# Optimization experiments

Measured on AMD Instinct MI355X. Metric: run time of the kernel, lower is better.

## Reference

```python
import jax, jax.numpy as jnp
import numpy as np

EPS = 1e-8  # torch.cosine_similarity clamps norms at eps=1e-8


def setup_inputs() -> dict:
    key = jax.random.key(0)
    k1, k2, k3 = jax.random.split(key, 3)
    B, C, D = 256, 128, 1024
    return {
        "doc_emb": jax.random.normal(k1, (B, D), dtype=jnp.float32),
        "summary_emb": jax.random.normal(k2, (B, D), dtype=jnp.float32),
        "candidate_emb": jax.random.normal(k3, (B, C, D), dtype=jnp.float32),
    }


def _clamped_norm(x):
    return jnp.maximum(jnp.linalg.norm(x, axis=-1), EPS)


def reference(doc_emb, summary_emb, candidate_emb):
    # doc_emb: [B, D], summary_emb: [B, D], candidate_emb: [B, C, D]
    B, C, D = candidate_emb.shape
    dn = _clamped_norm(doc_emb)          # [B]
    sn = _clamped_norm(summary_emb)      # [B]
    cn = _clamped_norm(candidate_emb)    # [B, C]

    # outer_score[b,c] = cos(candidate[b,c], doc[b])
    outer_score = jnp.einsum("bcd,bd->bc", candidate_emb, doc_emb) / (cn * dn[:, None])

    # inner_score: replaces the O(B*C^2) python loop with one batched Gram matmul.
    chat = candidate_emb / cn[:, :, None]           # unit candidates [B, C, D]
    gram = jnp.einsum("bcd,bkd->bck", chat, chat)    # [B, C, C] cosine sims
    diag = jnp.einsum("bcc->bc", gram)               # self-similarity (==1)
    inner_score = (gram.sum(axis=-1) - diag) / (C - 1)  # mean over _cn != cn

    # summary_score[b] = cos(summary[b], doc[b])
    summary_score = jnp.einsum("bd,bd->b", summary_emb, doc_emb) / (sn * dn)

    # summary_avg_score[b] = mean_c cos(summary[b], candidate[b,c])
    sc = jnp.einsum("bd,bcd->bc", summary_emb, candidate_emb) / (sn[:, None] * cn)
    summary_avg_score = sc.mean(axis=-1)

    return (outer_score, inner_score, summary_score, summary_avg_score)
```

## Files before the change

kernel.cpp:

```cpp
#include <hip/hip_runtime.h>
#include <math.h>


#define EPS 1e-8f
constexpr int B = 256;
constexpr int C = 128;
constexpr int D = 1024;

__device__ __forceinline__ float waveReduceSum(float v) {
    v += __shfl_down(v, 32, 64);
    v += __shfl_down(v, 16, 64);
    v += __shfl_down(v, 8, 64);
    v += __shfl_down(v, 4, 64);
    v += __shfl_down(v, 2, 64);
    v += __shfl_down(v, 1, 64);
    return v;
}

__global__ __launch_bounds__(256) void k0_norms(
    const float* __restrict__ doc, const float* __restrict__ summ,
    float* __restrict__ dn_inv, float* __restrict__ sn_inv,
    float* __restrict__ out_sumscore, float* __restrict__ out_sumavg) {
    const int b = blockIdx.x;
    const int t = threadIdx.x;
    const float4 dv = ((const float4*)(doc + (size_t)b * D))[t];
    const float4 sv = ((const float4*)(summ + (size_t)b * D))[t];
    float dd = dv.x * dv.x + dv.y * dv.y + dv.z * dv.z + dv.w * dv.w;
    float ss = sv.x * sv.x + sv.y * sv.y + sv.z * sv.z + sv.w * sv.w;
    float sd = sv.x * dv.x + sv.y * dv.y + sv.z * dv.z + sv.w * dv.w;
    dd = waveReduceSum(dd);
    ss = waveReduceSum(ss);
    sd = waveReduceSum(sd);
    __shared__ float red[3][4];
    const int wave = t >> 6, lane = t & 63;
    if (lane == 0) { red[0][wave] = dd; red[1][wave] = ss; red[2][wave] = sd; }
    __syncthreads();
    if (t == 0) {
        const float DD = red[0][0] + red[0][1] + red[0][2] + red[0][3];
        const float SS = red[1][0] + red[1][1] + red[1][2] + red[1][3];
        const float SD = red[2][0] + red[2][1] + red[2][2] + red[2][3];
        const float di = 1.0f / fmaxf(sqrtf(DD), EPS);
        const float si = 1.0f / fmaxf(sqrtf(SS), EPS);
        dn_inv[b] = di;
        sn_inv[b] = si;
        out_sumscore[b] = SD * di * si;
        out_sumavg[b] = 0.0f;
    }
}

__global__ __launch_bounds__(256) void k1_cand(
    const float* __restrict__ cand, const float* __restrict__ doc,
    const float* __restrict__ summ, const float* __restrict__ dn_inv,
    const float* __restrict__ sn_inv, float* __restrict__ inv_cn,
    float* __restrict__ out_outer, float* __restrict__ out_sumavg) {
    const int blk = blockIdx.x;
    const int b = blk >> 5;
    const int g = blk & 31;
    const int t = threadIdx.x;
    const int wave = t >> 6, lane = t & 63;
    const int c = g * 4 + wave;

    __shared__ float4 doc_s[D / 4];
    __shared__ float4 sum_s[D / 4];
    doc_s[t] = ((const float4*)(doc + (size_t)b * D))[t];
    sum_s[t] = ((const float4*)(summ + (size_t)b * D))[t];
    __syncthreads();

    const float4* cp = (const float4*)(cand + ((size_t)b * C + c) * D);
    float cd = 0.0f, cs = 0.0f, cc = 0.0f;
#pragma unroll
    for (int q = 0; q < 4; ++q) {
        const float4 cv = cp[lane + 64 * q];
        const float4 dv = doc_s[lane + 64 * q];
        const float4 sv = sum_s[lane + 64 * q];
        cd += cv.x * dv.x + cv.y * dv.y + cv.z * dv.z + cv.w * dv.w;
        cs += cv.x * sv.x + cv.y * sv.y + cv.z * sv.z + cv.w * sv.w;
        cc += cv.x * cv.x + cv.y * cv.y + cv.z * cv.z + cv.w * cv.w;
    }
    cd = waveReduceSum(cd);
    cs = waveReduceSum(cs);
    cc = waveReduceSum(cc);

    __shared__ float scs[4];
    if (lane == 0) {
        const float ic = 1.0f / fmaxf(sqrtf(cc), EPS);
        inv_cn[b * C + c] = ic;
        out_outer[b * C + c] = cd * ic * dn_inv[b];
        scs[wave] = cs * ic * sn_inv[b];
    }
    __syncthreads();
    if (t == 0) {
        atomicAdd(&out_sumavg[b],
                  (scs[0] + scs[1] + scs[2] + scs[3]) * (1.0f / C));
    }
}

__global__ __launch_bounds__(256) void k2_chatsum(
    const float* __restrict__ cand, const float* __restrict__ inv_cn,
    float* __restrict__ s) {
    const int b = blockIdx.x;
    const int t = threadIdx.x;
    __shared__ float ic[C];
    if (t < C) ic[t] = inv_cn[b * C + t];
    __syncthreads();
    const float4* cp = (const float4*)(cand + (size_t)b * C * D);
    float4 acc = make_float4(0.0f, 0.0f, 0.0f, 0.0f);
    for (int c = 0; c < C; ++c) {
        const float4 v = cp[c * (D / 4) + t];
        const float w = ic[c];
        acc.x += v.x * w;
        acc.y += v.y * w;
        acc.z += v.z * w;
        acc.w += v.w * w;
    }
    ((float4*)(s + (size_t)b * D))[t] = acc;
}

__global__ __launch_bounds__(256) void k3_inner(
    const float* __restrict__ cand, const float* __restrict__ s,
    const float* __restrict__ inv_cn, float* __restrict__ out_inner) {
    const int blk = blockIdx.x;
    const int b = blk >> 5;
    const int g = blk & 31;
    const int t = threadIdx.x;
    const int wave = t >> 6, lane = t & 63;
    const int c = g * 4 + wave;

    __shared__ float4 s_s[D / 4];
    s_s[t] = ((const float4*)(s + (size_t)b * D))[t];
    __syncthreads();

    const float4* cp = (const float4*)(cand + ((size_t)b * C + c) * D);
    float td = 0.0f;
#pragma unroll
    for (int q = 0; q < 4; ++q) {
        const float4 cv = cp[lane + 64 * q];
        const float4 sv = s_s[lane + 64 * q];
        td += cv.x * sv.x + cv.y * sv.y + cv.z * sv.z + cv.w * sv.w;
    }
    td = waveReduceSum(td);
    if (lane == 0) {
        out_inner[b * C + c] =
            (td * inv_cn[b * C + c] - 1.0f) * (1.0f / (C - 1));
    }
}

extern "C" void kernel_launch(void* const* d_in, const int* in_sizes, int n_in,
                              void* d_out, int out_size, void* d_ws,
                              size_t ws_size, hipStream_t stream) {
    const float* doc = (const float*)d_in[0];
    const float* summ = (const float*)d_in[1];
    const float* cand = (const float*)d_in[2];

    float* out = (float*)d_out;
    float* out_outer = out;
    float* out_inner = out + B * C;
    float* out_sumscore = out + 2 * B * C;
    float* out_sumavg = out + 2 * B * C + B;

    float* ws = (float*)d_ws;
    float* dn_inv = ws;
    float* sn_inv = ws + B;
    float* inv_cn = ws + 2 * B;
    float* s = ws + 2 * B + B * C;

    k0_norms<<<B, 256, 0, stream>>>(doc, summ, dn_inv, sn_inv, out_sumscore,
                                    out_sumavg);
    k1_cand<<<B * (C / 4), 256, 0, stream>>>(cand, doc, summ, dn_inv, sn_inv,
                                             inv_cn, out_outer, out_sumavg);
    k2_chatsum<<<B, 256, 0, stream>>>(cand, inv_cn, s);
    k3_inner<<<B * (C / 4), 256, 0, stream>>>(cand, s, inv_cn, out_inner);
}
```

Baseline: 238.8 us.

## Fuse norm, outer, chat-sum and inner passes into one per-batch kernel

Replaces four kernels with a single kernel where one 1024-thread block handles a batch row. Candidate norms, outer scores, summary averages and the normalized candidate sum are computed in one pass, with the sum reduced through LDS. A second pass over the same candidates computes inner scores, hoping they are still cache-resident. This removes the global workspace, the atomics and three launches, but uses only one block per batch, which limits parallelism and latency hiding.

```diff
diff --git a/kernel.cpp b/kernel.cpp
--- a/kernel.cpp
+++ b/kernel.cpp
@@ -6,142 +6,133 @@
 constexpr int B = 256;
 constexpr int C = 128;
 constexpr int D = 1024;
+constexpr int NW = 16;
+constexpr int CPW = C / NW;
 
-__device__ __forceinline__ float waveReduceSum(float v) {
-    v += __shfl_down(v, 32, 64);
-    v += __shfl_down(v, 16, 64);
-    v += __shfl_down(v, 8, 64);
-    v += __shfl_down(v, 4, 64);
-    v += __shfl_down(v, 2, 64);
-    v += __shfl_down(v, 1, 64);
+__device__ __forceinline__ float bflySum(float v) {
+    v += __shfl_xor(v, 1, 64);
+    v += __shfl_xor(v, 2, 64);
+    v += __shfl_xor(v, 4, 64);
+    v += __shfl_xor(v, 8, 64);
+    v += __shfl_xor(v, 16, 64);
+    v += __shfl_xor(v, 32, 64);
     return v;
 }
 
-__global__ __launch_bounds__(256) void k0_norms(
+__device__ __forceinline__ float dot4(const float4 a, const float4 b) {
+    return a.x * b.x + a.y * b.y + a.z * b.z + a.w * b.w;
+}
+
+__global__ __launch_bounds__(1024) void rerank_all(
     const float* __restrict__ doc, const float* __restrict__ summ,
-    float* __restrict__ dn_inv, float* __restrict__ sn_inv,
-    float* __restrict__ out_sumscore, float* __restrict__ out_sumavg) {
+    const float* __restrict__ cand, float* __restrict__ out_outer,
+    float* __restrict__ out_inner, float* __restrict__ out_sumscore,
+    float* __restrict__ out_sumavg) {
     const int b = blockIdx.x;
     const int t = threadIdx.x;
-    const float4 dv = ((const float4*)(doc + (size_t)b * D))[t];
-    const float4 sv = ((const float4*)(summ + (size_t)b * D))[t];
-    float dd = dv.x * dv.x + dv.y * dv.y + dv.z * dv.z + dv.w * dv.w;
-    float ss = sv.x * sv.x + sv.y * sv.y + sv.z * sv.z + sv.w * sv.w;
-    float sd = sv.x * dv.x + sv.y * dv.y + sv.z * dv.z + sv.w * dv.w;
-    dd = waveReduceSum(dd);
-    ss = waveReduceSum(ss);
-    sd = waveReduceSum(sd);
-    __shared__ float red[3][4];
-    const int wave = t >> 6, lane = t & 63;
-    if (lane == 0) { red[0][wave] = dd; red[1][wave] = ss; red[2][wave] = sd; }
-    __syncthreads();
-    if (t == 0) {
-        const float DD = red[0][0] + red[0][1] + red[0][2] + red[0][3];
-        const float SS = red[1][0] + red[1][1] + red[1][2] + red[1][3];
-        const float SD = red[2][0] + red[2][1] + red[2][2] + red[2][3];
-        const float di = 1.0f / fmaxf(sqrtf(DD), EPS);
-        const float si = 1.0f / fmaxf(sqrtf(SS), EPS);
-        dn_inv[b] = di;
-        sn_inv[b] = si;
-        out_sumscore[b] = SD * di * si;
-        out_sumavg[b] = 0.0f;
+    const int wave = t >> 6;
+    const int lane = t & 63;
+
+    __shared__ float s_part[NW][D];
+    __shared__ float s_full[D];
+    __shared__ float ic_lds[C];
+    __shared__ float sa_lds[NW];
+
+    const float4* dp = (const float4*)(doc + (size_t)b * D);
+    const float4* sp = (const float4*)(summ + (size_t)b * D);
+    float4 d4[4], m4[4];
+#pragma unroll
+    for (int q = 0; q < 4; ++q) {
+        d4[q] = dp[lane + 64 * q];
+        m4[q] = sp[lane + 64 * q];
     }
-}
+    float dd = 0.0f, ss = 0.0f, sd = 0.0f;
+#pragma unroll
+    for (int q = 0; q < 4; ++q) {
+        dd += dot4(d4[q], d4[q]);
+        ss += dot4(m4[q], m4[q]);
+        sd += dot4(m4[q], d4[q]);
+    }
+    dd = bflySum(dd);
+    ss = bflySum(ss);
+    sd = bflySum(sd);
+    const float di = 1.0f / fmaxf(sqrtf(dd), EPS);
+    const float si = 1.0f / fmaxf(sqrtf(ss), EPS);
+    if (t == 0) out_sumscore[b] = sd * di * si;
 
-__global__ __launch_bounds__(256) void k1_cand(
-    const float* __restrict__ cand, const float* __restrict__ doc,
-    const float* __restrict__ summ, const float* __restrict__ dn_inv,
-    const float* __restrict__ sn_inv, float* __restrict__ inv_cn,
-    float* __restrict__ out_outer, float* __restrict__ out_sumavg) {
-    const int blk = blockIdx.x;
-    const int b = blk >> 5;
-    const int g = blk & 31;
-    const int t = threadIdx.x;
-    const int wave = t >> 6, lane = t & 63;
-    const int c = g * 4 + wave;
+    const float4* cb = (const float4*)(cand + (size_t)b * C * D);
+    float4 s_prv[4];
+#pragma unroll
+    for (int q = 0; q < 4; ++q) s_prv[q] = make_float4(0.f, 0.f, 0.f, 0.f);
+    float sa_acc = 0.0f;
 
-    __shared__ float4 doc_s[D / 4];
-    __shared__ float4 sum_s[D / 4];
-    doc_s[t] = ((const float4*)(doc + (size_t)b * D))[t];
-    sum_s[t] = ((const float4*)(summ + (size_t)b * D))[t];
+#pragma unroll 2
+    for (int i = 0; i < CPW; ++i) {
+        const int c = wave * CPW + i;
+        const float4* cp = cb + (size_t)c * (D / 4);
+        float4 cv[4];
+#pragma unroll
+        for (int q = 0; q < 4; ++q) cv[q] = cp[lane + 64 * q];
+        float cc = 0.0f, cd = 0.0f, cs = 0.0f;
+#pragma unroll
+        for (int q = 0; q < 4; ++q) {
+            cc += dot4(cv[q], cv[q]);
+            cd += dot4(cv[q], d4[q]);
+            cs += dot4(cv[q], m4[q]);
+        }
+        cc = bflySum(cc);
+        cd = bflySum(cd);
+        cs = bflySum(cs);
+        const float icv = 1.0f / fmaxf(sqrtf(cc), EPS);
+        if (lane == 0) {
+            ic_lds[c] = icv;
+            out_outer[b * C + c] = cd * icv * di;
+        }
+        sa_acc += cs * icv;
+#pragma unroll
+        for (int q = 0; q < 4; ++q) {
+            s_prv[q].x += cv[q].x * icv;
+            s_prv[q].y += cv[q].y * icv;
+            s_prv[q].z += cv[q].z * icv;
+            s_prv[q].w += cv[q].w * icv;
+        }
+    }
+#pragma unroll
+    for (int q = 0; q < 4; ++q)
+        ((float4*)s_part[wave])[lane + 64 * q] = s_prv[q];
+    if (lane == 0) sa_lds[wave] = sa_acc;
     __syncthreads();
 
-    const float4* cp = (const float4*)(cand + ((size_t)b * C + c) * D);
-    float cd = 0.0f, cs = 0.0f, cc = 0.0f;
+    float colsum = 0.0f;
 #pragma unroll
-    for (int q = 0; q < 4; ++q) {
-        const float4 cv = cp[lane + 64 * q];
-        const float4 dv = doc_s[lane + 64 * q];
-        const float4 sv = sum_s[lane + 64 * q];
-        cd += cv.x * dv.x + cv.y * dv.y + cv.z * dv.z + cv.w * dv.w;
-        cs += cv.x * sv.x + cv.y * sv.y + cv.z * sv.z + cv.w * sv.w;
-        cc += cv.x * cv.x + cv.y * cv.y + cv.z * cv.z + cv.w * cv.w;
-    }
-    cd = waveReduceSum(cd);
-    cs = waveReduceSum(cs);
-    cc = waveReduceSum(cc);
-
-    __shared__ float scs[4];
-    if (lane == 0) {
-        const float ic = 1.0f / fmaxf(sqrtf(cc), EPS);
-        inv_cn[b * C + c] = ic;
-        out_outer[b * C + c] = cd * ic * dn_inv[b];
-        scs[wave] = cs * ic * sn_inv[b];
+    for (int w = 0; w < NW; ++w) colsum += s_part[w][t];
+    s_full[t] = colsum;
+    if (t == 0) {
+        float S = 0.0f;
+#pragma unroll
+        for (int w = 0; w < NW; ++w) S += sa_lds[w];
+        out_sumavg[b] = S * si * (1.0f / C);
     }
     __syncthreads();
-    if (t == 0) {
-        atomicAdd(&out_sumavg[b],
-                  (scs[0] + scs[1] + scs[2] + scs[3]) * (1.0f / C));
-    }
-}
 
-__global__ __launch_bounds__(256) void k2_chatsum(
-    const float* __restrict__ cand, const float* __restrict__ inv_cn,
-    float* __restrict__ s) {
-    const int b = blockIdx.x;
-    const int t = threadIdx.x;
-    __shared__ float ic[C];
-    if (t < C) ic[t] = inv_cn[b * C + t];
-    __syncthreads();
-    const float4* cp = (const float4*)(cand + (size_t)b * C * D);
-    float4 acc = make_float4(0.0f, 0.0f, 0.0f, 0.0f);
-    for (int c = 0; c < C; ++c) {
-        const float4 v = cp[c * (D / 4) + t];
-        const float w = ic[c];
-        acc.x += v.x * w;
-        acc.y += v.y * w;
-        acc.z += v.z * w;
-        acc.w += v.w * w;
-    }
-    ((float4*)(s + (size_t)b * D))[t] = acc;
-}
+    float4 s4[4];
+#pragma unroll
+    for (int q = 0; q < 4; ++q) s4[q] = ((const float4*)s_full)[lane + 64 * q];
 
-__global__ __launch_bounds__(256) void k3_inner(
-    const float* __restrict__ cand, const float* __restrict__ s,
-    const float* __restrict__ inv_cn, float* __restrict__ out_inner) {
-    const int blk = blockIdx.x;
-    const int b = blk >> 5;
-    const int g = blk & 31;
-    const int t = threadIdx.x;
-    const int wave = t >> 6, lane = t & 63;
-    const int c = g * 4 + wave;
-
-    __shared__ float4 s_s[D / 4];
-    s_s[t] = ((const float4*)(s + (size_t)b * D))[t];
-    __syncthreads();
-
-    const float4* cp = (const float4*)(cand + ((size_t)b * C + c) * D);
-    float td = 0.0f;
+#pragma unroll 2
+    for (int i = 0; i < CPW; ++i) {
+        const int c = wave * CPW + i;
+        const float4* cp = cb + (size_t)c * (D / 4);
+        float td = 0.0f;
 #pragma unroll
-    for (int q = 0; q < 4; ++q) {
-        const float4 cv = cp[lane + 64 * q];
-        const float4 sv = s_s[lane + 64 * q];
-        td += cv.x * sv.x + cv.y * sv.y + cv.z * sv.z + cv.w * sv.w;
-    }
-    td = waveReduceSum(td);
-    if (lane == 0) {
-        out_inner[b * C + c] =
-            (td * inv_cn[b * C + c] - 1.0f) * (1.0f / (C - 1));
+        for (int q = 0; q < 4; ++q) {
+            const float4 cv = cp[lane + 64 * q];
+            td += dot4(cv, s4[q]);
+        }
+        td = bflySum(td);
+        if (lane == 0)
+            out_inner[b * C + c] =
+                (td * ic_lds[c] - 1.0f) * (1.0f / (C - 1));
     }
 }
 
@@ -158,16 +149,6 @@
     float* out_sumscore = out + 2 * B * C;
     float* out_sumavg = out + 2 * B * C + B;
 
-    float* ws = (float*)d_ws;
-    float* dn_inv = ws;
-    float* sn_inv = ws + B;
-    float* inv_cn = ws + 2 * B;
-    float* s = ws + 2 * B + B * C;
-
-    k0_norms<<<B, 256, 0, stream>>>(doc, summ, dn_inv, sn_inv, out_sumscore,
-                                    out_sumavg);
-    k1_cand<<<B * (C / 4), 256, 0, stream>>>(cand, doc, summ, dn_inv, sn_inv,
-                                             inv_cn, out_outer, out_sumavg);
-    k2_chatsum<<<B, 256, 0, stream>>>(cand, inv_cn, s);
-    k3_inner<<<B * (C / 4), 256, 0, stream>>>(cand, s, inv_cn, out_inner);
+    rerank_all<<<B, 1024, 0, stream>>>(doc, summ, cand, out_outer, out_inner,
+                                       out_sumscore, out_sumavg);
 }
```

After: 213.9 us. 1.12x faster.
